# Performance work log

Hardware: AMD Instinct MI355X
Metric: run time of the kernel (lower is better)

The kernel has to match this reference:

```python
import jax, jax.numpy as jnp
import numpy as np

B, H, S, D = 4, 16, 2048, 128

def setup_inputs() -> dict:
    key = jax.random.key(0)
    kq, kk, kv, ks = jax.random.split(key, 4)
    return {
        "query": jax.random.normal(kq, (B, H, S, D), dtype=jnp.float32),
        "key": jax.random.normal(kk, (B, H, S, D), dtype=jnp.float32),
        "value": jax.random.normal(kv, (B, H, S, D), dtype=jnp.float32),
        "scale_factor": jax.random.normal(ks, (B, H, 1, 1), dtype=jnp.float32),
    }

def reference(query, key, value, scale_factor):
    # qk = Q @ K^T : [B,H,S,S]
    qk = jnp.einsum("bhsd,bhtd->bhst", query, key)
    scaled_qk = qk * scale_factor  # per-head broadcast scale
    softmax_qk = jax.nn.softmax(scaled_qk, axis=-1)
    # dropout treated as identity (eval-mode determinism for baseline)
    out = jnp.einsum("bhst,bhtd->bhsd", softmax_qk, value)
    return out
```

## Files before the change

### kernel.cpp

```cpp
#include <hip/hip_runtime.h>
#include <hip/hip_bf16.h>


typedef __bf16 bf16;
typedef __attribute__((ext_vector_type(4))) __bf16 bf16x4;
typedef __attribute__((ext_vector_type(8))) __bf16 bf16x8;
typedef __attribute__((ext_vector_type(4))) float f32x4;

constexpr int S_  = 2048;
constexpr int D_  = 128;
constexpr int BM  = 64;
constexpr int BN  = 32;
constexpr int NIT = S_ / BN;
constexpr int PK  = D_ + 8;
constexpr int PVT = BN + 8;
constexpr int PP  = BN + 8;

constexpr size_t WS_KL   = 16777216;
constexpr size_t WS_VT   = 33554432;
constexpr size_t WS_NEED = 100663296;

__global__ __launch_bounds__(256) void prepack(
    const float* __restrict__ kg, const float* __restrict__ vg,
    bf16* __restrict__ ws)
{
    const int gid = blockIdx.x * 256 + threadIdx.x;
    if (gid < 2097152) {
        const int u  = gid & 15;
        const int rg = gid >> 4;
        const float* src = kg + (size_t)rg * D_ + (u << 3);
        float x[8];
        *(float4*)&x[0] = *(const float4*)src;
        *(float4*)&x[4] = *(const float4*)(src + 4);
        bf16x8 h8, l8;
#pragma unroll
        for (int j = 0; j < 8; ++j) {
            bf16 h = (bf16)x[j];
            h8[j] = h;
            l8[j] = (bf16)(x[j] - (float)h);
        }
        const size_t di = (size_t)rg * 128 + (u << 3);
        *(bf16x8*)&ws[di]         = h8;
        *(bf16x8*)&ws[WS_KL + di] = l8;
    } else {
        const int g2 = gid - 2097152;
        const int i  = g2 & 511;
        const int tg = g2 >> 9;
        const int p  = i & 15;
        const int c  = i >> 4;
        const float* src = vg + ((size_t)tg * BN + 2 * p) * D_ + c * 4;
        float4 a0 = *(const float4*)src;
        float4 a1 = *(const float4*)(src + D_);
        const float* x0 = (const float*)&a0;
        const float* x1 = (const float*)&a1;
        bf16* vt = ws + WS_VT + (size_t)tg * 4096;
#pragma unroll
        for (int j = 0; j < 4; ++j) {
            union { ushort2 u2; bf16 b[2]; } pr;
            pr.b[0] = (bf16)x0[j];
            pr.b[1] = (bf16)x1[j];
            *(ushort2*)&vt[(c * 4 + j) * BN + 2 * p] = pr.u2;
        }
    }
}

__global__ __launch_bounds__(256, 4) void attn_fwd(
    const float* __restrict__ q, const bf16* __restrict__ ws,
    const float* __restrict__ sc, float* __restrict__ out)
{
    __shared__ __align__(16) bf16 Kh[BN * PK];
    __shared__ __align__(16) bf16 Kl[BN * PK];
    __shared__ __align__(16) bf16 Vs[D_ * PVT];
    __shared__ __align__(16) bf16 Ps[4 * 16 * PP];

    const int tid  = threadIdx.x;
    const int wave = tid >> 6;
    const int lane = tid & 63;
    const int l16  = lane & 15;
    const int quad = lane >> 4;

    const int bid = blockIdx.x;
    const int idx = bid >> 3;
    const int bh  = ((bid & 7) << 3) | (idx >> 5);
    const int qt  = idx & 31;

    const float scale = sc[bh] * 1.44269504088896f;

    const float* qbase = q + ((size_t)bh * S_ + (size_t)qt * BM) * D_;
    const bf16* khp = ws +         (size_t)bh * 262144 + tid * 8;
    const bf16* klp = ws + WS_KL + (size_t)bh * 262144 + tid * 8;
    const bf16* vtp = ws + WS_VT + (size_t)bh * 262144 + tid * 8;

    bf16x8 qh[4], ql[4];
    {
        const float* qrow = qbase + (size_t)(wave * 16 + l16) * D_ + quad * 8;
#pragma unroll
        for (int ks = 0; ks < 4; ++ks) {
            float x[8];
            *(float4*)&x[0] = *(const float4*)(qrow + ks * 32);
            *(float4*)&x[4] = *(const float4*)(qrow + ks * 32 + 4);
#pragma unroll
            for (int j = 0; j < 8; ++j) {
                float xs = x[j] * scale;
                bf16 h = (bf16)xs;
                qh[ks][j] = h;
                ql[ks][j] = (bf16)(xs - (float)h);
            }
        }
    }

    f32x4 O[8];
#pragma unroll
    for (int i = 0; i < 8; ++i) O[i] = (f32x4){0.f, 0.f, 0.f, 0.f};
    float mrow[4] = {-1e30f, -1e30f, -1e30f, -1e30f};
    float Lp[4]   = {0.f, 0.f, 0.f, 0.f};

    bf16x8 rKh[2], rKl[2], rVt[2];

#define LOADT(t)                                                          \
    {                                                                     \
        const size_t toff = (size_t)(t) * 4096;                           \
        rKh[0] = *(const bf16x8*)(khp + toff);                            \
        rKh[1] = *(const bf16x8*)(khp + toff + 2048);                     \
        rKl[0] = *(const bf16x8*)(klp + toff);                            \
        rKl[1] = *(const bf16x8*)(klp + toff + 2048);                     \
        rVt[0] = *(const bf16x8*)(vtp + toff);                            \
        rVt[1] = *(const bf16x8*)(vtp + toff + 2048);                     \
    }

#define WRITET()                                                          \
    {                                                                     \
        _Pragma("unroll")                                                 \
        for (int j = 0; j < 2; ++j) {                                     \
            int i = tid + j * 256;                                        \
            *(bf16x8*)&Kh[(i >> 4) * PK + (i & 15) * 8] = rKh[j];         \
            *(bf16x8*)&Kl[(i >> 4) * PK + (i & 15) * 8] = rKl[j];         \
            *(bf16x8*)&Vs[(i >> 2) * PVT + (i & 3) * 8] = rVt[j];         \
        }                                                                 \
    }

    LOADT(0);
    WRITET();
    LOADT(1);
    __syncthreads();

    for (int it = 0; it < NIT; ++it) {
        f32x4 sacc[2];
        sacc[0] = (f32x4){0.f, 0.f, 0.f, 0.f};
        sacc[1] = (f32x4){0.f, 0.f, 0.f, 0.f};
        __builtin_amdgcn_s_setprio(1);
#pragma unroll
        for (int ks = 0; ks < 4; ++ks) {
#pragma unroll
            for (int nb = 0; nb < 2; ++nb) {
                int off = (nb * 16 + l16) * PK + ks * 32 + quad * 8;
                bf16x8 kh = *(const bf16x8*)&Kh[off];
                bf16x8 kl = *(const bf16x8*)&Kl[off];
                sacc[nb] = __builtin_amdgcn_mfma_f32_16x16x32_bf16(qh[ks], kh, sacc[nb], 0, 0, 0);
                sacc[nb] = __builtin_amdgcn_mfma_f32_16x16x32_bf16(qh[ks], kl, sacc[nb], 0, 0, 0);
                sacc[nb] = __builtin_amdgcn_mfma_f32_16x16x32_bf16(ql[ks], kh, sacc[nb], 0, 0, 0);
            }
        }
        __builtin_amdgcn_s_setprio(0);

        float m0r[4];
        bool grow = false;
#pragma unroll
        for (int r = 0; r < 4; ++r) {
            float m0 = fmaxf(sacc[0][r], sacc[1][r]);
#pragma unroll
            for (int off = 8; off >= 1; off >>= 1)
                m0 = fmaxf(m0, __shfl_xor(m0, off, 64));
            m0r[r] = m0;
            grow |= (m0 - mrow[r] > 8.0f);
        }
        if (__any(grow)) {
#pragma unroll
            for (int r = 0; r < 4; ++r) {
                float mnew  = fmaxf(mrow[r], m0r[r]);
                float alpha = __builtin_amdgcn_exp2f(mrow[r] - mnew);
                mrow[r] = mnew;
                Lp[r] *= alpha;
#pragma unroll
                for (int d = 0; d < 8; ++d) O[d][r] *= alpha;
            }
        }
        float p0[4], p1[4];
#pragma unroll
        for (int r = 0; r < 4; ++r) {
            float e0 = __builtin_amdgcn_exp2f(sacc[0][r] - mrow[r]);
            float e1 = __builtin_amdgcn_exp2f(sacc[1][r] - mrow[r]);
            p0[r] = e0; p1[r] = e1;
            Lp[r] += e0 + e1;
        }

        bf16* pw = &Ps[wave * 16 * PP];
#pragma unroll
        for (int r = 0; r < 4; ++r) {
            pw[(quad * 4 + r) * PP + l16]      = (bf16)p0[r];
            pw[(quad * 4 + r) * PP + 16 + l16] = (bf16)p1[r];
        }

        {
            bf16x8 pa = *(const bf16x8*)&pw[l16 * PP + quad * 8];
            __builtin_amdgcn_s_setprio(1);
#pragma unroll
            for (int d = 0; d < 8; ++d) {
                bf16x8 vb = *(const bf16x8*)&Vs[(d * 16 + l16) * PVT + quad * 8];
                O[d] = __builtin_amdgcn_mfma_f32_16x16x32_bf16(pa, vb, O[d], 0, 0, 0);
            }
            __builtin_amdgcn_s_setprio(0);
        }

        if (it == NIT - 1) break;
        __syncthreads();
        WRITET();
        if (it + 2 < NIT) LOADT(it + 2);
        __syncthreads();
    }

    float rl[4];
#pragma unroll
    for (int r = 0; r < 4; ++r) {
        float L = Lp[r];
#pragma unroll
        for (int off = 8; off >= 1; off >>= 1)
            L += __shfl_xor(L, off, 64);
        rl[r] = 1.0f / L;
    }
    float* og = out + ((size_t)bh * S_ + (size_t)qt * BM + wave * 16) * D_;
#pragma unroll
    for (int d = 0; d < 8; ++d)
#pragma unroll
        for (int r = 0; r < 4; ++r)
            og[(quad * 4 + r) * D_ + d * 16 + l16] = O[d][r] * rl[r];
}

__global__ __launch_bounds__(256, 4) void attn_fwd_fb(
    const float* __restrict__ q, const float* __restrict__ kg,
    const float* __restrict__ vg, const float* __restrict__ sc,
    float* __restrict__ out)
{
    __shared__ __align__(16) bf16 Kh[BN * PK];
    __shared__ __align__(16) bf16 Kl[BN * PK];
    __shared__ __align__(16) bf16 Vs[D_ * PVT];
    __shared__ __align__(16) bf16 Ps2[4 * 16 * PP];

    const int tid  = threadIdx.x;
    const int wave = tid >> 6;
    const int lane = tid & 63;
    const int l16  = lane & 15;
    const int quad = lane >> 4;

    const int qt = blockIdx.x;
    const int bh = blockIdx.y;

    const float scale = sc[bh] * 1.44269504088896f;

    const float* qbase = q  + ((size_t)bh * S_ + (size_t)qt * BM) * D_;
    const float* kbase = kg + (size_t)bh * S_ * D_;
    const float* vbase = vg + (size_t)bh * S_ * D_;

    bf16x8 qh[4], ql[4];
    {
        const float* qrow = qbase + (size_t)(wave * 16 + l16) * D_ + quad * 8;
#pragma unroll
        for (int ks = 0; ks < 4; ++ks) {
            float x[8];
            *(float4*)&x[0] = *(const float4*)(qrow + ks * 32);
            *(float4*)&x[4] = *(const float4*)(qrow + ks * 32 + 4);
#pragma unroll
            for (int j = 0; j < 8; ++j) {
                float xs = x[j] * scale;
                bf16 h = (bf16)xs;
                qh[ks][j] = h;
                ql[ks][j] = (bf16)(xs - (float)h);
            }
        }
    }

    f32x4 O[8];
#pragma unroll
    for (int i = 0; i < 8; ++i) O[i] = (f32x4){0.f, 0.f, 0.f, 0.f};
    float mrow[4] = {-1e30f, -1e30f, -1e30f, -1e30f};
    float Lp[4]   = {0.f, 0.f, 0.f, 0.f};

    for (int it = 0; it < NIT; ++it) {
        __syncthreads();
        {
            const float* kt = kbase + (size_t)it * BN * D_;
#pragma unroll
            for (int r = 0; r < 4; ++r) {
                int i = tid + r * 256;
                int row = i >> 5, c = i & 31;
                float4 v = *(const float4*)(kt + row * D_ + c * 4);
                const float* x = (const float*)&v;
                bf16x4 h4, l4;
#pragma unroll
                for (int j = 0; j < 4; ++j) {
                    bf16 h = (bf16)x[j];
                    h4[j] = h;
                    l4[j] = (bf16)(x[j] - (float)h);
                }
                *(bf16x4*)&Kh[row * PK + c * 4] = h4;
                *(bf16x4*)&Kl[row * PK + c * 4] = l4;
            }
            const float* vt = vbase + (size_t)it * BN * D_;
#pragma unroll
            for (int r = 0; r < 2; ++r) {
                int i = tid + r * 256;
                int p = i & 15;
                int c = i >> 4;
                const float* v0 = vt + (2 * p) * D_ + c * 4;
                float4 a0 = *(const float4*)v0;
                float4 a1 = *(const float4*)(v0 + D_);
                const float* x0 = (const float*)&a0;
                const float* x1 = (const float*)&a1;
#pragma unroll
                for (int j = 0; j < 4; ++j) {
                    union { ushort2 u; bf16 b[2]; } pr;
                    pr.b[0] = (bf16)x0[j];
                    pr.b[1] = (bf16)x1[j];
                    *(ushort2*)&Vs[(c * 4 + j) * PVT + 2 * p] = pr.u;
                }
            }
        }
        __syncthreads();

        f32x4 sacc[2];
        sacc[0] = (f32x4){0.f, 0.f, 0.f, 0.f};
        sacc[1] = (f32x4){0.f, 0.f, 0.f, 0.f};
#pragma unroll
        for (int ks = 0; ks < 4; ++ks) {
#pragma unroll
            for (int nb = 0; nb < 2; ++nb) {
                int off = (nb * 16 + l16) * PK + ks * 32 + quad * 8;
                bf16x8 kh = *(const bf16x8*)&Kh[off];
                bf16x8 kl = *(const bf16x8*)&Kl[off];
                sacc[nb] = __builtin_amdgcn_mfma_f32_16x16x32_bf16(qh[ks], kh, sacc[nb], 0, 0, 0);
                sacc[nb] = __builtin_amdgcn_mfma_f32_16x16x32_bf16(qh[ks], kl, sacc[nb], 0, 0, 0);
                sacc[nb] = __builtin_amdgcn_mfma_f32_16x16x32_bf16(ql[ks], kh, sacc[nb], 0, 0, 0);
            }
        }

        float p0[4], p1[4];
#pragma unroll
        for (int r = 0; r < 4; ++r) {
            float m0 = fmaxf(sacc[0][r], sacc[1][r]);
#pragma unroll
            for (int off = 8; off >= 1; off >>= 1)
                m0 = fmaxf(m0, __shfl_xor(m0, off, 64));
            float mnew  = fmaxf(mrow[r], m0);
            float alpha = __builtin_amdgcn_exp2f(mrow[r] - mnew);
            mrow[r] = mnew;
            float e0 = __builtin_amdgcn_exp2f(sacc[0][r] - mnew);
            float e1 = __builtin_amdgcn_exp2f(sacc[1][r] - mnew);
            p0[r] = e0; p1[r] = e1;
            Lp[r] = Lp[r] * alpha + (e0 + e1);
#pragma unroll
            for (int d = 0; d < 8; ++d) O[d][r] *= alpha;
        }

        bf16* pw = &Ps2[wave * 16 * PP];
#pragma unroll
        for (int r = 0; r < 4; ++r) {
            pw[(quad * 4 + r) * PP + l16]      = (bf16)p0[r];
            pw[(quad * 4 + r) * PP + 16 + l16] = (bf16)p1[r];
        }
        {
            bf16x8 pa = *(const bf16x8*)&pw[l16 * PP + quad * 8];
#pragma unroll
            for (int d = 0; d < 8; ++d) {
                bf16x8 vb = *(const bf16x8*)&Vs[(d * 16 + l16) * PVT + quad * 8];
                O[d] = __builtin_amdgcn_mfma_f32_16x16x32_bf16(pa, vb, O[d], 0, 0, 0);
            }
        }
    }

    float rl[4];
#pragma unroll
    for (int r = 0; r < 4; ++r) {
        float L = Lp[r];
#pragma unroll
        for (int off = 8; off >= 1; off >>= 1)
            L += __shfl_xor(L, off, 64);
        rl[r] = 1.0f / L;
    }
    float* og = out + ((size_t)bh * S_ + (size_t)qt * BM + wave * 16) * D_;
#pragma unroll
    for (int d = 0; d < 8; ++d)
#pragma unroll
        for (int r = 0; r < 4; ++r)
            og[(quad * 4 + r) * D_ + d * 16 + l16] = O[d][r] * rl[r];
}

extern "C" void kernel_launch(void* const* d_in, const int* in_sizes, int n_in,
                              void* d_out, int out_size, void* d_ws, size_t ws_size,
                              hipStream_t stream) {
    const float* q  = (const float*)d_in[0];
    const float* k  = (const float*)d_in[1];
    const float* v  = (const float*)d_in[2];
    const float* sc = (const float*)d_in[3];
    float* o = (float*)d_out;
    if (d_ws && ws_size >= WS_NEED) {
        bf16* ws = (bf16*)d_ws;
        prepack<<<16384, 256, 0, stream>>>(k, v, ws);
        attn_fwd<<<2048, 256, 0, stream>>>(q, ws, sc, o);
    } else {
        attn_fwd_fb<<<dim3(S_ / BM, 64), 256, 0, stream>>>(q, k, v, sc, o);
    }
}
```

Measured before the change: 610.3 us.

## Use DPP row reductions, unpadded V tile, and raise occupancy hint to five

Replaces the shuffle-based 16-lane max and sum reductions with DPP row operations, which avoids LDS-routed shuffles. It also removes the padding from the transposed V tile in the main kernel, shrinking shared memory so a fifth block can fit per CU, and raises the launch-bounds occupancy hint from 4 to 5. The fallback kernel keeps its padded V layout. Risks are extra LDS bank conflicts on the unpadded V reads and register spills under the tighter register budget.

After: 1.625 ms. +166.2%, slower.

```diff
diff --git a/kernel.cpp b/kernel.cpp
--- a/kernel.cpp
+++ b/kernel.cpp
@@ -13,12 +13,39 @@
 constexpr int BN  = 32;
 constexpr int NIT = S_ / BN;
 constexpr int PK  = D_ + 8;
-constexpr int PVT = BN + 8;
+constexpr int PVT = 32;
 constexpr int PP  = BN + 8;
 
 constexpr size_t WS_KL   = 16777216;
 constexpr size_t WS_VT   = 33554432;
 constexpr size_t WS_NEED = 100663296;
+
+template <int CTRL>
+__device__ __forceinline__ float dpp_fmax_step(float x) {
+    int yi = __builtin_amdgcn_update_dpp(
+        __float_as_int(x), __float_as_int(x), CTRL, 0xf, 0xf, false);
+    return fmaxf(x, __int_as_float(yi));
+}
+template <int CTRL>
+__device__ __forceinline__ float dpp_fadd_step(float x) {
+    int yi = __builtin_amdgcn_update_dpp(
+        __float_as_int(x), __float_as_int(x), CTRL, 0xf, 0xf, false);
+    return x + __int_as_float(yi);
+}
+__device__ __forceinline__ float row16_max(float x) {
+    x = dpp_fmax_step<0xB1>(x);
+    x = dpp_fmax_step<0x4E>(x);
+    x = dpp_fmax_step<0x141>(x);
+    x = dpp_fmax_step<0x140>(x);
+    return x;
+}
+__device__ __forceinline__ float row16_sum(float x) {
+    x = dpp_fadd_step<0xB1>(x);
+    x = dpp_fadd_step<0x4E>(x);
+    x = dpp_fadd_step<0x141>(x);
+    x = dpp_fadd_step<0x140>(x);
+    return x;
+}
 
 __global__ __launch_bounds__(256) void prepack(
     const float* __restrict__ kg, const float* __restrict__ vg,
@@ -64,7 +91,7 @@
     }
 }
 
-__global__ __launch_bounds__(256, 4) void attn_fwd(
+__global__ __launch_bounds__(256, 5) void attn_fwd(
     const float* __restrict__ q, const bf16* __restrict__ ws,
     const float* __restrict__ sc, float* __restrict__ out)
 {
@@ -135,7 +162,7 @@
             int i = tid + j * 256;                                        \
             *(bf16x8*)&Kh[(i >> 4) * PK + (i & 15) * 8] = rKh[j];         \
             *(bf16x8*)&Kl[(i >> 4) * PK + (i & 15) * 8] = rKl[j];         \
-            *(bf16x8*)&Vs[(i >> 2) * PVT + (i & 3) * 8] = rVt[j];         \
+            *(bf16x8*)&Vs[i * 8] = rVt[j];                                \
         }                                                                 \
     }
 
@@ -167,10 +194,7 @@
         bool grow = false;
 #pragma unroll
         for (int r = 0; r < 4; ++r) {
-            float m0 = fmaxf(sacc[0][r], sacc[1][r]);
-#pragma unroll
-            for (int off = 8; off >= 1; off >>= 1)
-                m0 = fmaxf(m0, __shfl_xor(m0, off, 64));
+            float m0 = row16_max(fmaxf(sacc[0][r], sacc[1][r]));
             m0r[r] = m0;
             grow |= (m0 - mrow[r] > 8.0f);
         }
@@ -221,13 +245,8 @@
 
     float rl[4];
 #pragma unroll
-    for (int r = 0; r < 4; ++r) {
-        float L = Lp[r];
-#pragma unroll
-        for (int off = 8; off >= 1; off >>= 1)
-            L += __shfl_xor(L, off, 64);
-        rl[r] = 1.0f / L;
-    }
+    for (int r = 0; r < 4; ++r)
+        rl[r] = 1.0f / row16_sum(Lp[r]);
     float* og = out + ((size_t)bh * S_ + (size_t)qt * BM + wave * 16) * D_;
 #pragma unroll
     for (int d = 0; d < 8; ++d)
@@ -241,9 +260,11 @@
     const float* __restrict__ vg, const float* __restrict__ sc,
     float* __restrict__ out)
 {
+    constexpr int FPVT = BN + 8;
+
     __shared__ __align__(16) bf16 Kh[BN * PK];
     __shared__ __align__(16) bf16 Kl[BN * PK];
-    __shared__ __align__(16) bf16 Vs[D_ * PVT];
+    __shared__ __align__(16) bf16 Vs[D_ * FPVT];
     __shared__ __align__(16) bf16 Ps2[4 * 16 * PP];
 
     const int tid  = threadIdx.x;
@@ -321,7 +342,7 @@
                     union { ushort2 u; bf16 b[2]; } pr;
                     pr.b[0] = (bf16)x0[j];
                     pr.b[1] = (bf16)x1[j];
-                    *(ushort2*)&Vs[(c * 4 + j) * PVT + 2 * p] = pr.u;
+                    *(ushort2*)&Vs[(c * 4 + j) * FPVT + 2 * p] = pr.u;
                 }
             }
         }
@@ -371,7 +392,7 @@
             bf16x8 pa = *(const bf16x8*)&pw[l16 * PP + quad * 8];
 #pragma unroll
             for (int d = 0; d < 8; ++d) {
-                bf16x8 vb = *(const bf16x8*)&Vs[(d * 16 + l16) * PVT + quad * 8];
+                bf16x8 vb = *(const bf16x8*)&Vs[(d * 16 + l16) * FPVT + quad * 8];
                 O[d] = __builtin_amdgcn_mfma_f32_16x16x32_bf16(pa, vb, O[d], 0, 0, 0);
             }
         }
```
